# Optimization experiments

Hardware: AMD Instinct MI355X
Metric: run time of the kernel (lower is better)

## Reference

```python
import jax, jax.numpy as jnp
import numpy as np
from jax import lax

DIM = 256
HEAD_DIM = 64          # v head dim and hedgehog dim
HEAD_DIM_QK = 64       # must equal HEAD_DIM for the module to run
NH = DIM // HEAD_DIM   # 4
EPS = 1e-6


def setup_inputs() -> dict:
    key = jax.random.key(0)
    ks = jax.random.split(key, 12)
    B, C, H, W, D = 1, DIM, 16, 16, 16
    x = jax.random.normal(ks[0], (B, C, H, W, D), dtype=jnp.float32)
    qk_dim = HEAD_DIM_QK * NH
    # 1x1x1 conv weights for q, k (qkv_bias=False)
    Wq = jax.random.normal(ks[1], (qk_dim, C), dtype=jnp.float32) * 0.02
    Wk = jax.random.normal(ks[2], (qk_dim, C), dtype=jnp.float32) * 0.02
    # depthwise 3x3x3 conv for v (groups=dim, bias=True)
    Wv = jax.random.normal(ks[3], (C, 1, 3, 3, 3), dtype=jnp.float32) * 0.1
    bv = jax.random.normal(ks[4], (C,), dtype=jnp.float32) * 0.02
    # HedgeHog linear layers (init is identity/zeros; use near-identity + noise)
    eye = jnp.eye(HEAD_DIM, dtype=jnp.float32)
    Wmq = eye * 0.5 + jax.random.normal(ks[5], (HEAD_DIM, HEAD_DIM), dtype=jnp.float32) * 0.02
    bmq = jnp.zeros((HEAD_DIM,), dtype=jnp.float32)
    Wmk = eye * 0.5 + jax.random.normal(ks[6], (HEAD_DIM, HEAD_DIM), dtype=jnp.float32) * 0.02
    bmk = jnp.zeros((HEAD_DIM,), dtype=jnp.float32)
    Wmv = eye * 0.5 + jax.random.normal(ks[7], (HEAD_DIM, HEAD_DIM), dtype=jnp.float32) * 0.02
    bmv = jnp.zeros((HEAD_DIM,), dtype=jnp.float32)
    return {"x": x, "Wq": Wq, "Wk": Wk, "Wv": Wv, "bv": bv,
            "Wmq": Wmq, "bmq": bmq, "Wmk": Wmk, "bmk": bmk,
            "Wmv": Wmv, "bmv": bmv}


def _hedgehog(z, W, b):
    # z: [B, nh, N, d] -> [B, 2*nh, N, d]; cat along HEAD axis (dim=1) as in torch code
    h = jnp.einsum('bhnd,ed->bhne', z, W) + b
    return jnp.concatenate([jnp.exp(h), jnp.exp(-h)], axis=1)


def reference(x, Wq, Wk, Wv, bv, Wmq, bmq, Wmk, bmk, Wmv, bmv):
    B, C, H, W_, D = x.shape
    N = H * W_ * D
    x2 = x.reshape(B, C, N)
    # 1x1x1 conv projections
    q = jnp.einsum('oc,bcn->bon', Wq, x2)  # [B, qk_dim, N]
    k = jnp.einsum('oc,bcn->bon', Wk, x2)
    # depthwise 3x3x3 conv for v
    v3 = lax.conv_general_dilated(
        x, Wv, window_strides=(1, 1, 1),
        padding=((1, 1), (1, 1), (1, 1)),
        dimension_numbers=('NCDHW', 'OIDHW', 'NCDHW'),
        feature_group_count=C) + bv[None, :, None, None, None]
    v = v3.reshape(B, C, N)
    # split heads, tokens-last -> tokens axis
    q1 = q.reshape(B, NH, HEAD_DIM_QK, N).transpose(0, 1, 3, 2)  # [B,nh,N,dqk]
    k1 = k.reshape(B, NH, HEAD_DIM_QK, N).transpose(0, 1, 3, 2)
    v1 = v.reshape(B, NH, HEAD_DIM, N).transpose(0, 1, 3, 2)     # [B,nh,N,dv]
    qf = _hedgehog(q1, Wmq, bmq)  # [B,2nh,N,dqk]
    kf = _hedgehog(k1, Wmk, bmk)
    vf = _hedgehog(v1, Wmv, bmv)  # [B,2nh,N,dv]
    # quadratic "linear" attention: row-sum normalized QK^T
    qk = jnp.einsum('bhmd,bhnd->bhmn', qf, kf)          # [B,2nh,N,N]
    attn = qk / (jnp.sum(qk, axis=-1, keepdims=True) + EPS)
    out = jnp.einsum('bhmn,bhnd->bhmd', attn, vf)        # [B,2nh,N,dv]
    out = out.transpose(0, 1, 3, 2).reshape(B, 2 * C, H, W_, D)
    return out
```

## Files before the change

### kernel.cpp

```cpp
#include <hip/hip_runtime.h>
#include <math.h>

#define EPS_F 1e-6f

#define OFF_WCQ 0
#define OFF_WCK (OFF_WCQ + 65536)
#define OFF_BV  (OFF_WCK + 65536)
#define OFF_VC  (OFF_BV + 256)
#define OFF_PS  (OFF_VC + 256*4096)
#define OFF_PSV (OFF_PS + 8*64*4096)
#define OFF_SM  (OFF_PSV + 8*64*64)
#define OFF_SV  (OFF_SM + 8*4096)

__global__ __launch_bounds__(256) void k_combine(
    const float* __restrict__ Wq, const float* __restrict__ Wk,
    const float* __restrict__ Wmq, const float* __restrict__ Wmk,
    const float* __restrict__ Wmv, const float* __restrict__ bmv,
    const float* __restrict__ bv, float* __restrict__ ws)
{
    int row = blockIdx.x;
    int c = threadIdx.x;
    int h = row >> 6, e = row & 63;
    float aq = 0.f, ak = 0.f;
    for (int d = 0; d < 64; ++d) {
        float mq = Wmq[e*64 + d];
        float mk = Wmk[e*64 + d];
        int src = (h*64 + d)*256 + c;
        aq = fmaf(mq, Wq[src], aq);
        ak = fmaf(mk, Wk[src], ak);
    }
    ws[OFF_WCQ + row*256 + c] = aq;
    ws[OFF_WCK + row*256 + c] = ak;
    if (c == 0) {
        float av = 0.f;
        for (int d = 0; d < 64; ++d) av = fmaf(Wmv[e*64 + d], bv[h*64 + d], av);
        ws[OFF_BV + row] = av + bmv[e];
    }
}

__global__ __launch_bounds__(256) void k_dwconv(
    const float* __restrict__ x, const float* __restrict__ Wv, float* __restrict__ vc)
{
    int c = blockIdx.y;
    int n = blockIdx.x * 256 + threadIdx.x;
    int z = n >> 8, y = (n >> 4) & 15, xx = n & 15;
    const float* xc = x + c * 4096;
    const float* wc = Wv + c * 27;
    float acc = 0.f;
    #pragma unroll
    for (int kz = 0; kz < 3; ++kz) {
        int zz = z + kz - 1;
        if (zz < 0 || zz > 15) continue;
        #pragma unroll
        for (int ky = 0; ky < 3; ++ky) {
            int yy = y + ky - 1;
            if (yy < 0 || yy > 15) continue;
            #pragma unroll
            for (int kx = 0; kx < 3; ++kx) {
                int xv = xx + kx - 1;
                if (xv < 0 || xv > 15) continue;
                acc = fmaf(wc[(kz*3 + ky)*3 + kx], xc[(zz << 8) + (yy << 4) + xv], acc);
            }
        }
    }
    vc[c*4096 + n] = acc;
}

__global__ __launch_bounds__(256, 1) void k_kv_fused(
    const float* __restrict__ X, const float* __restrict__ bmk,
    const float* __restrict__ Wmv, float* __restrict__ ws)
{
    __shared__ float smem[16384];
    float (*Xs)[64]  = (float(*)[64])smem;
    float (*Ws)[68]  = (float(*)[68])(smem + 4096);
    float (*kfp)[64] = (float(*)[64])smem;
    float (*kfm)[64] = (float(*)[64])(smem + 4096);
    float (*vfp)[64] = (float(*)[64])(smem + 8192);
    float (*vfm)[64] = (float(*)[64])(smem + 12288);

    int t = threadIdx.x;
    int chunk = blockIdx.x;
    int hb = blockIdx.y;
    int n0 = chunk * 64;
    int lc = t >> 6, ln = t & 63;
    int e4 = (t & 15) * 4;
    int n4 = (t >> 4) * 4;

    float accK[4][4], accV[4][4];
    #pragma unroll
    for (int i = 0; i < 4; ++i)
        #pragma unroll
        for (int j = 0; j < 4; ++j) { accK[i][j] = 0.f; accV[i][j] = 0.f; }

    const float* Wck = ws + OFF_WCK;
    for (int c0 = 0; c0 < 256; c0 += 64) {
        #pragma unroll
        for (int i = 0; i < 16; ++i)
            Xs[lc*16 + i][ln] = X[(size_t)(c0 + lc*16 + i)*4096 + n0 + ln];
        #pragma unroll
        for (int i = 0; i < 16; ++i)
            Ws[ln][lc*16 + i] = Wck[(size_t)(hb*64 + lc*16 + i)*256 + c0 + ln];
        __syncthreads();
        #pragma unroll 4
        for (int c = 0; c < 64; ++c) {
            float4 xv4 = *(const float4*)&Xs[c][n4];
            float4 wv4 = *(const float4*)&Ws[c][e4];
            float xv[4] = {xv4.x, xv4.y, xv4.z, xv4.w};
            float wv[4] = {wv4.x, wv4.y, wv4.z, wv4.w};
            #pragma unroll
            for (int ii = 0; ii < 4; ++ii)
                #pragma unroll
                for (int jj = 0; jj < 4; ++jj)
                    accK[ii][jj] = fmaf(xv[ii], wv[jj], accK[ii][jj]);
        }
        __syncthreads();
    }

    const float* vcb = ws + OFF_VC + (size_t)hb*64*4096;
    #pragma unroll
    for (int i = 0; i < 16; ++i)
        Xs[lc*16 + i][ln] = vcb[(size_t)(lc*16 + i)*4096 + n0 + ln];
    #pragma unroll
    for (int i = 0; i < 16; ++i) { int idx = i*256 + t; Ws[idx & 63][idx >> 6] = Wmv[idx]; }
    __syncthreads();
    #pragma unroll 4
    for (int d = 0; d < 64; ++d) {
        float4 xv4 = *(const float4*)&Xs[d][n4];
        float4 wv4 = *(const float4*)&Ws[d][e4];
        float xv[4] = {xv4.x, xv4.y, xv4.z, xv4.w};
        float wv[4] = {wv4.x, wv4.y, wv4.z, wv4.w};
        #pragma unroll
        for (int ii = 0; ii < 4; ++ii)
            #pragma unroll
            for (int jj = 0; jj < 4; ++jj)
                accV[ii][jj] = fmaf(xv[ii], wv[jj], accV[ii][jj]);
    }
    __syncthreads();

    float bk[4], bvv[4];
    #pragma unroll
    for (int j = 0; j < 4; ++j) { bk[j] = bmk[e4 + j]; bvv[j] = ws[OFF_BV + hb*64 + e4 + j]; }
    #pragma unroll
    for (int ii = 0; ii < 4; ++ii) {
        float pk[4], mk_[4], pv[4], mv[4];
        #pragma unroll
        for (int jj = 0; jj < 4; ++jj) {
            float a = accK[ii][jj] + bk[jj];
            pk[jj] = __expf(a);  mk_[jj] = __expf(-a);
            float b = accV[ii][jj] + bvv[jj];
            pv[jj] = __expf(b);  mv[jj] = __expf(-b);
        }
        *(float4*)&kfp[n4 + ii][e4] = make_float4(pk[0], pk[1], pk[2], pk[3]);
        *(float4*)&kfm[n4 + ii][e4] = make_float4(mk_[0], mk_[1], mk_[2], mk_[3]);
        *(float4*)&vfp[n4 + ii][e4] = make_float4(pv[0], pv[1], pv[2], pv[3]);
        *(float4*)&vfm[n4 + ii][e4] = make_float4(mv[0], mv[1], mv[2], mv[3]);
    }
    __syncthreads();

    float aSp[4][4], aSm[4][4], svp[4], svm[4];
    #pragma unroll
    for (int i = 0; i < 4; ++i) {
        svp[i] = 0.f; svm[i] = 0.f;
        #pragma unroll
        for (int j = 0; j < 4; ++j) { aSp[i][j] = 0.f; aSm[i][j] = 0.f; }
    }
    int a4 = e4, f4 = n4;
    #pragma unroll 2
    for (int n = 0; n < 64; ++n) {
        float4 kp4 = *(const float4*)&kfp[n][a4];
        float4 km4 = *(const float4*)&kfm[n][a4];
        float4 vp4 = *(const float4*)&vfp[n][f4];
        float4 vm4 = *(const float4*)&vfm[n][f4];
        float kp[4] = {kp4.x, kp4.y, kp4.z, kp4.w};
        float km[4] = {km4.x, km4.y, km4.z, km4.w};
        float vp[4] = {vp4.x, vp4.y, vp4.z, vp4.w};
        float vm[4] = {vm4.x, vm4.y, vm4.z, vm4.w};
        #pragma unroll
        for (int ai = 0; ai < 4; ++ai) {
            svp[ai] += kp[ai];  svm[ai] += km[ai];
            #pragma unroll
            for (int fi = 0; fi < 4; ++fi) {
                aSp[ai][fi] = fmaf(kp[ai], vp[fi], aSp[ai][fi]);
                aSm[ai][fi] = fmaf(km[ai], vm[fi], aSm[ai][fi]);
            }
        }
    }
    float* pSp = ws + OFF_PS + (size_t)(hb*64 + chunk)*4096;
    float* pSm = ws + OFF_PS + (size_t)((hb + 4)*64 + chunk)*4096;
    #pragma unroll
    for (int ai = 0; ai < 4; ++ai) {
        *(float4*)&pSp[(a4 + ai)*64 + f4] = make_float4(aSp[ai][0], aSp[ai][1], aSp[ai][2], aSp[ai][3]);
        *(float4*)&pSm[(a4 + ai)*64 + f4] = make_float4(aSm[ai][0], aSm[ai][1], aSm[ai][2], aSm[ai][3]);
    }
    if (t < 16) {
        float* pvp = ws + OFF_PSV + (size_t)(hb*64 + chunk)*64;
        float* pvm = ws + OFF_PSV + (size_t)((hb + 4)*64 + chunk)*64;
        *(float4*)&pvp[a4] = make_float4(svp[0], svp[1], svp[2], svp[3]);
        *(float4*)&pvm[a4] = make_float4(svm[0], svm[1], svm[2], svm[3]);
    }
}

__global__ __launch_bounds__(256) void k_reduce(float* __restrict__ ws)
{
    int idx = blockIdx.x*256 + threadIdx.x;
    if (idx < 8*4096) {
        int h = idx >> 12, r = idx & 4095;
        float s = 0.f;
        #pragma unroll 16
        for (int c = 0; c < 64; ++c) s += ws[OFF_PS + (size_t)(h*64 + c)*4096 + r];
        ws[OFF_SM + idx] = s;
    } else if (idx < 8*4096 + 512) {
        int j = idx - 8*4096;
        int h = j >> 6, e = j & 63;
        float s = 0.f;
        #pragma unroll 16
        for (int c = 0; c < 64; ++c) s += ws[OFF_PSV + (size_t)(h*64 + c)*64 + e];
        ws[OFF_SV + j] = s;
    }
}

__global__ __launch_bounds__(256, 1) void k_q_out(
    const float* __restrict__ X, const float* __restrict__ bmq,
    const float* __restrict__ ws, float* __restrict__ out)
{
    __shared__ float smem[12352];
    float (*Xs)[64]   = (float(*)[64])smem;
    float (*Wsh)[68]  = (float(*)[68])(smem + 4096);
    float (*qfTp)[64] = (float(*)[64])smem;
    float (*qfTm)[64] = (float(*)[64])(smem + 4096);
    float (*Sms)[64]  = (float(*)[64])(smem + 8192);
    float* svs        = smem + 12288;

    int t = threadIdx.x;
    int chunk = blockIdx.x;
    int hb = blockIdx.y;
    int n0 = chunk * 64;
    int lc = t >> 6, ln = t & 63;
    int a4_1 = (t & 15) * 4;
    int n4_1 = (t >> 4) * 4;

    float accQ[4][4];
    #pragma unroll
    for (int i = 0; i < 4; ++i)
        #pragma unroll
        for (int j = 0; j < 4; ++j) accQ[i][j] = 0.f;

    const float* Wcq = ws + OFF_WCQ;
    for (int c0 = 0; c0 < 256; c0 += 64) {
        #pragma unroll
        for (int i = 0; i < 16; ++i)
            Xs[lc*16 + i][ln] = X[(size_t)(c0 + lc*16 + i)*4096 + n0 + ln];
        #pragma unroll
        for (int i = 0; i < 16; ++i)
            Wsh[ln][lc*16 + i] = Wcq[(size_t)(hb*64 + lc*16 + i)*256 + c0 + ln];
        __syncthreads();
        #pragma unroll 4
        for (int c = 0; c < 64; ++c) {
            float4 xv4 = *(const float4*)&Xs[c][n4_1];
            float4 wv4 = *(const float4*)&Wsh[c][a4_1];
            float xv[4] = {xv4.x, xv4.y, xv4.z, xv4.w};
            float wv[4] = {wv4.x, wv4.y, wv4.z, wv4.w};
            #pragma unroll
            for (int ii = 0; ii < 4; ++ii)
                #pragma unroll
                for (int jj = 0; jj < 4; ++jj)
                    accQ[ii][jj] = fmaf(xv[ii], wv[jj], accQ[ii][jj]);
        }
        __syncthreads();
    }

    #pragma unroll
    for (int jj = 0; jj < 4; ++jj) {
        float b = bmq[a4_1 + jj];
        float v0 = accQ[0][jj] + b, v1 = accQ[1][jj] + b,
              v2 = accQ[2][jj] + b, v3 = accQ[3][jj] + b;
        *(float4*)&qfTp[a4_1 + jj][n4_1] =
            make_float4(__expf(v0), __expf(v1), __expf(v2), __expf(v3));
        *(float4*)&qfTm[a4_1 + jj][n4_1] =
            make_float4(__expf(-v0), __expf(-v1), __expf(-v2), __expf(-v3));
    }

    int n4 = (t & 15) * 4;
    int e4 = (t >> 4) * 4;
    for (int s = 0; s < 2; ++s) {
        int h = hb + 4*s;
        __syncthreads();
        const float* Smg = ws + OFF_SM + (size_t)h*4096;
        #pragma unroll
        for (int i = 0; i < 16; ++i) { int idx = i*256 + t; Sms[idx >> 6][idx & 63] = Smg[idx]; }
        if (t < 64) svs[t] = ws[OFF_SV + h*64 + t];
        __syncthreads();

        const float (*qf)[64] = s ? (const float(*)[64])qfTm : (const float(*)[64])qfTp;
        float acc[4][4];
        float den[4] = {0.f, 0.f, 0.f, 0.f};
        #pragma unroll
        for (int i = 0; i < 4; ++i)
            #pragma unroll
            for (int j = 0; j < 4; ++j) acc[i][j] = 0.f;
        #pragma unroll 4
        for (int a = 0; a < 64; ++a) {
            float4 qv4 = *(const float4*)&qf[a][n4];
            float4 sm4 = *(const float4*)&Sms[a][e4];
            float qv[4] = {qv4.x, qv4.y, qv4.z, qv4.w};
            float sm[4] = {sm4.x, sm4.y, sm4.z, sm4.w};
            float sva = svs[a];
            #pragma unroll
            for (int nj = 0; nj < 4; ++nj) {
                den[nj] = fmaf(qv[nj], sva, den[nj]);
                #pragma unroll
                for (int ei = 0; ei < 4; ++ei)
                    acc[ei][nj] = fmaf(sm[ei], qv[nj], acc[ei][nj]);
            }
        }
        float r[4];
        #pragma unroll
        for (int nj = 0; nj < 4; ++nj) r[nj] = 1.f / (den[nj] + EPS_F);
        #pragma unroll
        for (int ei = 0; ei < 4; ++ei)
            *(float4*)&out[(size_t)(h*64 + e4 + ei)*4096 + n0 + n4] =
                make_float4(acc[ei][0]*r[0], acc[ei][1]*r[1], acc[ei][2]*r[2], acc[ei][3]*r[3]);
    }
}

extern "C" void kernel_launch(void* const* d_in, const int* in_sizes, int n_in,
                              void* d_out, int out_size, void* d_ws, size_t ws_size,
                              hipStream_t stream) {
    const float* x   = (const float*)d_in[0];
    const float* Wq  = (const float*)d_in[1];
    const float* Wk  = (const float*)d_in[2];
    const float* Wv  = (const float*)d_in[3];
    const float* bv  = (const float*)d_in[4];
    const float* Wmq = (const float*)d_in[5];
    const float* bmq = (const float*)d_in[6];
    const float* Wmk = (const float*)d_in[7];
    const float* bmk = (const float*)d_in[8];
    const float* Wmv = (const float*)d_in[9];
    const float* bmv = (const float*)d_in[10];
    float* out = (float*)d_out;
    float* ws  = (float*)d_ws;

    k_combine<<<256, 256, 0, stream>>>(Wq, Wk, Wmq, Wmk, Wmv, bmv, bv, ws);
    k_dwconv<<<dim3(16, 256), 256, 0, stream>>>(x, Wv, ws + OFF_VC);
    k_kv_fused<<<dim3(64, 4), 256, 0, stream>>>(x, bmk, Wmv, ws);
    k_reduce<<<130, 256, 0, stream>>>(ws);
    k_q_out<<<dim3(64, 4), 256, 0, stream>>>(x, bmq, ws, out);
}
```

Measured before the change: 147.0 us.

## Halve token chunk to double block count and stage dwconv planes in LDS

The token chunk per block in the KV and Q/output kernels drops from 64 to 32, doubling the grid to 128x4 blocks. Thread tiles and shared-memory layouts are reworked to match, with padded 68-wide rows and the min-blocks launch bound removed. The depthwise conv now stages three z-planes in shared memory and uses branchless clamped reads. The aim is to fill more of the many CUs, since 256 blocks underuse the GPU. In exchange the reduce kernel sums twice as many partial S matrices, and each block gets less register reuse.

```diff
diff --git a/kernel.cpp b/kernel.cpp
--- a/kernel.cpp
+++ b/kernel.cpp
@@ -2,14 +2,15 @@
 #include <math.h>
 
 #define EPS_F 1e-6f
+#define NCHUNK 128
 
 #define OFF_WCQ 0
 #define OFF_WCK (OFF_WCQ + 65536)
 #define OFF_BV  (OFF_WCK + 65536)
 #define OFF_VC  (OFF_BV + 256)
 #define OFF_PS  (OFF_VC + 256*4096)
-#define OFF_PSV (OFF_PS + 8*64*4096)
-#define OFF_SM  (OFF_PSV + 8*64*64)
+#define OFF_PSV (OFF_PS + 8*NCHUNK*4096)
+#define OFF_SM  (OFF_PSV + 8*NCHUNK*64)
 #define OFF_SV  (OFF_SM + 8*4096)
 
 __global__ __launch_bounds__(256) void k_combine(
@@ -41,74 +42,85 @@
 __global__ __launch_bounds__(256) void k_dwconv(
     const float* __restrict__ x, const float* __restrict__ Wv, float* __restrict__ vc)
 {
+    __shared__ float pl[3][256];
+    int t = threadIdx.x;
+    int z = blockIdx.x;
     int c = blockIdx.y;
-    int n = blockIdx.x * 256 + threadIdx.x;
-    int z = n >> 8, y = (n >> 4) & 15, xx = n & 15;
-    const float* xc = x + c * 4096;
-    const float* wc = Wv + c * 27;
-    float acc = 0.f;
+    const float* xc = x + (size_t)c*4096;
     #pragma unroll
     for (int kz = 0; kz < 3; ++kz) {
         int zz = z + kz - 1;
-        if (zz < 0 || zz > 15) continue;
+        pl[kz][t] = (zz >= 0 && zz < 16) ? xc[zz*256 + t] : 0.f;
+    }
+    __syncthreads();
+    int y = t >> 4, xx = t & 15;
+    const float* wc = Wv + c*27;
+    float acc = 0.f;
+    #pragma unroll
+    for (int kz = 0; kz < 3; ++kz) {
         #pragma unroll
         for (int ky = 0; ky < 3; ++ky) {
             int yy = y + ky - 1;
-            if (yy < 0 || yy > 15) continue;
+            bool vy = (yy >= 0) && (yy < 16);
+            int yc = yy < 0 ? 0 : (yy > 15 ? 15 : yy);
             #pragma unroll
             for (int kx = 0; kx < 3; ++kx) {
                 int xv = xx + kx - 1;
-                if (xv < 0 || xv > 15) continue;
-                acc = fmaf(wc[(kz*3 + ky)*3 + kx], xc[(zz << 8) + (yy << 4) + xv], acc);
+                bool v = vy && (xv >= 0) && (xv < 16);
+                int xc2 = xv < 0 ? 0 : (xv > 15 ? 15 : xv);
+                float val = pl[kz][yc*16 + xc2];
+                acc = fmaf(wc[(kz*3 + ky)*3 + kx], v ? val : 0.f, acc);
             }
         }
     }
-    vc[c*4096 + n] = acc;
-}
-
-__global__ __launch_bounds__(256, 1) void k_kv_fused(
+    vc[(size_t)c*4096 + z*256 + t] = acc;
+}
+
+__global__ __launch_bounds__(256) void k_kv_fused(
     const float* __restrict__ X, const float* __restrict__ bmk,
     const float* __restrict__ Wmv, float* __restrict__ ws)
 {
-    __shared__ float smem[16384];
-    float (*Xs)[64]  = (float(*)[64])smem;
-    float (*Ws)[68]  = (float(*)[68])(smem + 4096);
-    float (*kfp)[64] = (float(*)[64])smem;
-    float (*kfm)[64] = (float(*)[64])(smem + 4096);
-    float (*vfp)[64] = (float(*)[64])(smem + 8192);
-    float (*vfm)[64] = (float(*)[64])(smem + 12288);
+    __shared__ float smem[8704];
+    float* Xs  = smem;
+    float* Wsh = smem + 2048;
+    float* kfp = smem;
+    float* kfm = smem + 2176;
+    float* vfp = smem + 4352;
+    float* vfm = smem + 6528;
 
     int t = threadIdx.x;
     int chunk = blockIdx.x;
     int hb = blockIdx.y;
-    int n0 = chunk * 64;
+    int n0 = chunk * 32;
+    int e4 = (t & 15) * 4;
+    int n2 = (t >> 4) * 2;
     int lc = t >> 6, ln = t & 63;
-    int e4 = (t & 15) * 4;
-    int n4 = (t >> 4) * 4;
-
-    float accK[4][4], accV[4][4];
-    #pragma unroll
-    for (int i = 0; i < 4; ++i)
+
+    float accK[2][4], accV[2][4];
+    #pragma unroll
+    for (int i = 0; i < 2; ++i)
         #pragma unroll
         for (int j = 0; j < 4; ++j) { accK[i][j] = 0.f; accV[i][j] = 0.f; }
 
     const float* Wck = ws + OFF_WCK;
     for (int c0 = 0; c0 < 256; c0 += 64) {
         #pragma unroll
+        for (int i = 0; i < 8; ++i) {
+            int idx = i*256 + t, cc = idx >> 5, nn = idx & 31;
+            Xs[cc*32 + nn] = X[(size_t)(c0 + cc)*4096 + n0 + nn];
+        }
+        #pragma unroll
         for (int i = 0; i < 16; ++i)
-            Xs[lc*16 + i][ln] = X[(size_t)(c0 + lc*16 + i)*4096 + n0 + ln];
-        #pragma unroll
-        for (int i = 0; i < 16; ++i)
-            Ws[ln][lc*16 + i] = Wck[(size_t)(hb*64 + lc*16 + i)*256 + c0 + ln];
-        __syncthreads();
-        #pragma unroll 4
+            Wsh[ln*68 + lc*16 + i] = Wck[(size_t)(hb*64 + lc*16 + i)*256 + c0 + ln];
+        __syncthreads();
+        #pragma unroll 8
         for (int c = 0; c < 64; ++c) {
-            float4 xv4 = *(const float4*)&Xs[c][n4];
-            float4 wv4 = *(const float4*)&Ws[c][e4];
-            float xv[4] = {xv4.x, xv4.y, xv4.z, xv4.w};
+            float2 xv2 = *(const float2*)&Xs[c*32 + n2];
+            float4 wv4 = *(const float4*)&Wsh[c*68 + e4];
+            float xv[2] = {xv2.x, xv2.y};
             float wv[4] = {wv4.x, wv4.y, wv4.z, wv4.w};
             #pragma unroll
-            for (int ii = 0; ii < 4; ++ii)
+            for (int ii = 0; ii < 2; ++ii)
                 #pragma unroll
                 for (int jj = 0; jj < 4; ++jj)
                     accK[ii][jj] = fmaf(xv[ii], wv[jj], accK[ii][jj]);
@@ -116,32 +128,39 @@
         __syncthreads();
     }
 
-    const float* vcb = ws + OFF_VC + (size_t)hb*64*4096;
-    #pragma unroll
-    for (int i = 0; i < 16; ++i)
-        Xs[lc*16 + i][ln] = vcb[(size_t)(lc*16 + i)*4096 + n0 + ln];
-    #pragma unroll
-    for (int i = 0; i < 16; ++i) { int idx = i*256 + t; Ws[idx & 63][idx >> 6] = Wmv[idx]; }
-    __syncthreads();
-    #pragma unroll 4
-    for (int d = 0; d < 64; ++d) {
-        float4 xv4 = *(const float4*)&Xs[d][n4];
-        float4 wv4 = *(const float4*)&Ws[d][e4];
-        float xv[4] = {xv4.x, xv4.y, xv4.z, xv4.w};
-        float wv[4] = {wv4.x, wv4.y, wv4.z, wv4.w};
-        #pragma unroll
-        for (int ii = 0; ii < 4; ++ii)
-            #pragma unroll
-            for (int jj = 0; jj < 4; ++jj)
-                accV[ii][jj] = fmaf(xv[ii], wv[jj], accV[ii][jj]);
-    }
-    __syncthreads();
+    {
+        const float* vcb = ws + OFF_VC + (size_t)hb*64*4096;
+        #pragma unroll
+        for (int i = 0; i < 8; ++i) {
+            int idx = i*256 + t, dd = idx >> 5, nn = idx & 31;
+            Xs[dd*32 + nn] = vcb[(size_t)dd*4096 + n0 + nn];
+        }
+        #pragma unroll
+        for (int i = 0; i < 16; ++i) {
+            int idx = i*256 + t, dd = idx & 63, ee = idx >> 6;
+            Wsh[dd*68 + ee] = Wmv[ee*64 + dd];
+        }
+        __syncthreads();
+        #pragma unroll 8
+        for (int d = 0; d < 64; ++d) {
+            float2 xv2 = *(const float2*)&Xs[d*32 + n2];
+            float4 wv4 = *(const float4*)&Wsh[d*68 + e4];
+            float xv[2] = {xv2.x, xv2.y};
+            float wv[4] = {wv4.x, wv4.y, wv4.z, wv4.w};
+            #pragma unroll
+            for (int ii = 0; ii < 2; ++ii)
+                #pragma unroll
+                for (int jj = 0; jj < 4; ++jj)
+                    accV[ii][jj] = fmaf(xv[ii], wv[jj], accV[ii][jj]);
+        }
+        __syncthreads();
+    }
 
     float bk[4], bvv[4];
     #pragma unroll
     for (int j = 0; j < 4; ++j) { bk[j] = bmk[e4 + j]; bvv[j] = ws[OFF_BV + hb*64 + e4 + j]; }
     #pragma unroll
-    for (int ii = 0; ii < 4; ++ii) {
+    for (int ii = 0; ii < 2; ++ii) {
         float pk[4], mk_[4], pv[4], mv[4];
         #pragma unroll
         for (int jj = 0; jj < 4; ++jj) {
@@ -150,13 +169,15 @@
             float b = accV[ii][jj] + bvv[jj];
             pv[jj] = __expf(b);  mv[jj] = __expf(-b);
         }
-        *(float4*)&kfp[n4 + ii][e4] = make_float4(pk[0], pk[1], pk[2], pk[3]);
-        *(float4*)&kfm[n4 + ii][e4] = make_float4(mk_[0], mk_[1], mk_[2], mk_[3]);
-        *(float4*)&vfp[n4 + ii][e4] = make_float4(pv[0], pv[1], pv[2], pv[3]);
-        *(float4*)&vfm[n4 + ii][e4] = make_float4(mv[0], mv[1], mv[2], mv[3]);
+        int r = (n2 + ii)*68 + e4;
+        *(float4*)&kfp[r] = make_float4(pk[0], pk[1], pk[2], pk[3]);
+        *(float4*)&kfm[r] = make_float4(mk_[0], mk_[1], mk_[2], mk_[3]);
+        *(float4*)&vfp[r] = make_float4(pv[0], pv[1], pv[2], pv[3]);
+        *(float4*)&vfm[r] = make_float4(mv[0], mv[1], mv[2], mv[3]);
     }
     __syncthreads();
 
+    int a4 = e4, f4 = (t >> 4) * 4;
     float aSp[4][4], aSm[4][4], svp[4], svm[4];
     #pragma unroll
     for (int i = 0; i < 4; ++i) {
@@ -164,13 +185,12 @@
         #pragma unroll
         for (int j = 0; j < 4; ++j) { aSp[i][j] = 0.f; aSm[i][j] = 0.f; }
     }
-    int a4 = e4, f4 = n4;
-    #pragma unroll 2
-    for (int n = 0; n < 64; ++n) {
-        float4 kp4 = *(const float4*)&kfp[n][a4];
-        float4 km4 = *(const float4*)&kfm[n][a4];
-        float4 vp4 = *(const float4*)&vfp[n][f4];
-        float4 vm4 = *(const float4*)&vfm[n][f4];
+    #pragma unroll 4
+    for (int n = 0; n < 32; ++n) {
+        float4 kp4 = *(const float4*)&kfp[n*68 + a4];
+        float4 km4 = *(const float4*)&kfm[n*68 + a4];
+        float4 vp4 = *(const float4*)&vfp[n*68 + f4];
+        float4 vm4 = *(const float4*)&vfm[n*68 + f4];
         float kp[4] = {kp4.x, kp4.y, kp4.z, kp4.w};
         float km[4] = {km4.x, km4.y, km4.z, km4.w};
         float vp[4] = {vp4.x, vp4.y, vp4.z, vp4.w};
@@ -185,16 +205,16 @@
             }
         }
     }
-    float* pSp = ws + OFF_PS + (size_t)(hb*64 + chunk)*4096;
-    float* pSm = ws + OFF_PS + (size_t)((hb + 4)*64 + chunk)*4096;
+    float* pSp = ws + OFF_PS + (size_t)(hb*NCHUNK + chunk)*4096;
+    float* pSm = ws + OFF_PS + (size_t)((hb + 4)*NCHUNK + chunk)*4096;
     #pragma unroll
     for (int ai = 0; ai < 4; ++ai) {
         *(float4*)&pSp[(a4 + ai)*64 + f4] = make_float4(aSp[ai][0], aSp[ai][1], aSp[ai][2], aSp[ai][3]);
         *(float4*)&pSm[(a4 + ai)*64 + f4] = make_float4(aSm[ai][0], aSm[ai][1], aSm[ai][2], aSm[ai][3]);
     }
     if (t < 16) {
-        float* pvp = ws + OFF_PSV + (size_t)(hb*64 + chunk)*64;
-        float* pvm = ws + OFF_PSV + (size_t)((hb + 4)*64 + chunk)*64;
+        float* pvp = ws + OFF_PSV + (size_t)(hb*NCHUNK + chunk)*64;
+        float* pvm = ws + OFF_PSV + (size_t)((hb + 4)*NCHUNK + chunk)*64;
         *(float4*)&pvp[a4] = make_float4(svp[0], svp[1], svp[2], svp[3]);
         *(float4*)&pvm[a4] = make_float4(svm[0], svm[1], svm[2], svm[3]);
     }
@@ -206,120 +226,121 @@
     if (idx < 8*4096) {
         int h = idx >> 12, r = idx & 4095;
         float s = 0.f;
-        #pragma unroll 16
-        for (int c = 0; c < 64; ++c) s += ws[OFF_PS + (size_t)(h*64 + c)*4096 + r];
+        #pragma unroll 8
+        for (int c = 0; c < NCHUNK; ++c) s += ws[OFF_PS + (size_t)(h*NCHUNK + c)*4096 + r];
         ws[OFF_SM + idx] = s;
     } else if (idx < 8*4096 + 512) {
         int j = idx - 8*4096;
         int h = j >> 6, e = j & 63;
         float s = 0.f;
-        #pragma unroll 16
-        for (int c = 0; c < 64; ++c) s += ws[OFF_PSV + (size_t)(h*64 + c)*64 + e];
+        #pragma unroll 8
+        for (int c = 0; c < NCHUNK; ++c) s += ws[OFF_PSV + (size_t)(h*NCHUNK + c)*64 + e];
         ws[OFF_SV + j] = s;
     }
 }
 
-__global__ __launch_bounds__(256, 1) void k_q_out(
+__global__ __launch_bounds__(256) void k_q_out(
     const float* __restrict__ X, const float* __restrict__ bmq,
     const float* __restrict__ ws, float* __restrict__ out)
 {
-    __shared__ float smem[12352];
-    float (*Xs)[64]   = (float(*)[64])smem;
-    float (*Wsh)[68]  = (float(*)[68])(smem + 4096);
-    float (*qfTp)[64] = (float(*)[64])smem;
-    float (*qfTm)[64] = (float(*)[64])(smem + 4096);
-    float (*Sms)[64]  = (float(*)[64])(smem + 8192);
-    float* svs        = smem + 12288;
+    __shared__ float smem[8768];
+    float* Xs  = smem;
+    float* Wsh = smem + 2048;
+    float* qfp = smem;
+    float* qfm = smem + 2176;
+    float* Sms = smem + 4352;
+    float* svs = smem + 8704;
 
     int t = threadIdx.x;
     int chunk = blockIdx.x;
     int hb = blockIdx.y;
-    int n0 = chunk * 64;
+    int n0 = chunk * 32;
+    int e2 = (t & 31) * 2;
+    int n4 = (t >> 5) * 4;
     int lc = t >> 6, ln = t & 63;
-    int a4_1 = (t & 15) * 4;
-    int n4_1 = (t >> 4) * 4;
-
-    float accQ[4][4];
-    #pragma unroll
-    for (int i = 0; i < 4; ++i)
-        #pragma unroll
-        for (int j = 0; j < 4; ++j) accQ[i][j] = 0.f;
+
+    float accQ[4][2];
+    #pragma unroll
+    for (int i = 0; i < 4; ++i) { accQ[i][0] = 0.f; accQ[i][1] = 0.f; }
 
     const float* Wcq = ws + OFF_WCQ;
     for (int c0 = 0; c0 < 256; c0 += 64) {
         #pragma unroll
+        for (int i = 0; i < 8; ++i) {
+            int idx = i*256 + t, cc = idx >> 5, nn = idx & 31;
+            Xs[cc*32 + nn] = X[(size_t)(c0 + cc)*4096 + n0 + nn];
+        }
+        #pragma unroll
         for (int i = 0; i < 16; ++i)
-            Xs[lc*16 + i][ln] = X[(size_t)(c0 + lc*16 + i)*4096 + n0 + ln];
-        #pragma unroll
-        for (int i = 0; i < 16; ++i)
-            Wsh[ln][lc*16 + i] = Wcq[(size_t)(hb*64 + lc*16 + i)*256 + c0 + ln];
-        __syncthreads();
-        #pragma unroll 4
+            Wsh[ln*68 + lc*16 + i] = Wcq[(size_t)(hb*64 + lc*16 + i)*256 + c0 + ln];
+        __syncthreads();
+        #pragma unroll 8
         for (int c = 0; c < 64; ++c) {
-            float4 xv4 = *(const float4*)&Xs[c][n4_1];
-            float4 wv4 = *(const float4*)&Wsh[c][a4_1];
+            float4 xv4 = *(const float4*)&Xs[c*32 + n4];
+            float2 wv2 = *(const float2*)&Wsh[c*68 + e2];
             float xv[4] = {xv4.x, xv4.y, xv4.z, xv4.w};
-            float wv[4] = {wv4.x, wv4.y, wv4.z, wv4.w};
+            float wv[2] = {wv2.x, wv2.y};
             #pragma unroll
             for (int ii = 0; ii < 4; ++ii)
                 #pragma unroll
-                for (int jj = 0; jj < 4; ++jj)
+                for (int jj = 0; jj < 2; ++jj)
                     accQ[ii][jj] = fmaf(xv[ii], wv[jj], accQ[ii][jj]);
         }
         __syncthreads();
     }
 
-    #pragma unroll
-    for (int jj = 0; jj < 4; ++jj) {
-        float b = bmq[a4_1 + jj];
-        float v0 = accQ[0][jj] + b, v1 = accQ[1][jj] + b,
-              v2 = accQ[2][jj] + b, v3 = accQ[3][jj] + b;
-        *(float4*)&qfTp[a4_1 + jj][n4_1] =
-            make_float4(__expf(v0), __expf(v1), __expf(v2), __expf(v3));
-        *(float4*)&qfTm[a4_1 + jj][n4_1] =
-            make_float4(__expf(-v0), __expf(-v1), __expf(-v2), __expf(-v3));
-    }
-
-    int n4 = (t & 15) * 4;
-    int e4 = (t >> 4) * 4;
+    float bq[2] = {bmq[e2], bmq[e2 + 1]};
+    #pragma unroll
+    for (int ii = 0; ii < 4; ++ii) {
+        float a0 = accQ[ii][0] + bq[0];
+        float a1 = accQ[ii][1] + bq[1];
+        int r = (n4 + ii)*68 + e2;
+        *(float2*)&qfp[r] = make_float2(__expf(a0),  __expf(a1));
+        *(float2*)&qfm[r] = make_float2(__expf(-a0), __expf(-a1));
+    }
+
     for (int s = 0; s < 2; ++s) {
         int h = hb + 4*s;
         __syncthreads();
         const float* Smg = ws + OFF_SM + (size_t)h*4096;
         #pragma unroll
-        for (int i = 0; i < 16; ++i) { int idx = i*256 + t; Sms[idx >> 6][idx & 63] = Smg[idx]; }
+        for (int i = 0; i < 16; ++i) {
+            int idx = i*256 + t;
+            Sms[(idx >> 6)*68 + (idx & 63)] = Smg[idx];
+        }
         if (t < 64) svs[t] = ws[OFF_SV + h*64 + t];
         __syncthreads();
 
-        const float (*qf)[64] = s ? (const float(*)[64])qfTm : (const float(*)[64])qfTp;
-        float acc[4][4];
+        const float* qf = s ? qfm : qfp;
+        float accO[2][4];
         float den[4] = {0.f, 0.f, 0.f, 0.f};
         #pragma unroll
-        for (int i = 0; i < 4; ++i)
-            #pragma unroll
-            for (int j = 0; j < 4; ++j) acc[i][j] = 0.f;
+        for (int j = 0; j < 2; ++j)
+            #pragma unroll
+            for (int i = 0; i < 4; ++i) accO[j][i] = 0.f;
         #pragma unroll 4
         for (int a = 0; a < 64; ++a) {
-            float4 qv4 = *(const float4*)&qf[a][n4];
-            float4 sm4 = *(const float4*)&Sms[a][e4];
-            float qv[4] = {qv4.x, qv4.y, qv4.z, qv4.w};
-            float sm[4] = {sm4.x, sm4.y, sm4.z, sm4.w};
             float sva = svs[a];
-            #pragma unroll
-            for (int nj = 0; nj < 4; ++nj) {
-                den[nj] = fmaf(qv[nj], sva, den[nj]);
+            float2 sm2 = *(const float2*)&Sms[a*68 + e2];
+            float sm[2] = {sm2.x, sm2.y};
+            float qv[4];
+            #pragma unroll
+            for (int i = 0; i < 4; ++i) qv[i] = qf[(n4 + i)*68 + a];
+            #pragma unroll
+            for (int i = 0; i < 4; ++i) {
+                den[i] = fmaf(qv[i], sva, den[i]);
                 #pragma unroll
-                for (int ei = 0; ei < 4; ++ei)
-                    acc[ei][nj] = fmaf(sm[ei], qv[nj], acc[ei][nj]);
+                for (int j = 0; j < 2; ++j)
+                    accO[j][i] = fmaf(sm[j], qv[i], accO[j][i]);
             }
         }
         float r[4];
         #pragma unroll
-        for (int nj = 0; nj < 4; ++nj) r[nj] = 1.f / (den[nj] + EPS_F);
-        #pragma unroll
-        for (int ei = 0; ei < 4; ++ei)
-            *(float4*)&out[(size_t)(h*64 + e4 + ei)*4096 + n0 + n4] =
-                make_float4(acc[ei][0]*r[0], acc[ei][1]*r[1], acc[ei][2]*r[2], acc[ei][3]*r[3]);
+        for (int i = 0; i < 4; ++i) r[i] = 1.f / (den[i] + EPS_F);
+        #pragma unroll
+        for (int j = 0; j < 2; ++j)
+            *(float4*)&out[(size_t)(h*64 + e2 + j)*4096 + n0 + n4] =
+                make_float4(accO[j][0]*r[0], accO[j][1]*r[1], accO[j][2]*r[2], accO[j][3]*r[3]);
     }
 }
 
@@ -342,7 +363,7 @@
 
     k_combine<<<256, 256, 0, stream>>>(Wq, Wk, Wmq, Wmk, Wmv, bmv, bv, ws);
     k_dwconv<<<dim3(16, 256), 256, 0, stream>>>(x, Wv, ws + OFF_VC);
-    k_kv_fused<<<dim3(64, 4), 256, 0, stream>>>(x, bmk, Wmv, ws);
+    k_kv_fused<<<dim3(NCHUNK, 4), 256, 0, stream>>>(x, bmk, Wmv, ws);
     k_reduce<<<130, 256, 0, stream>>>(ws);
-    k_q_out<<<dim3(64, 4), 256, 0, stream>>>(x, bmq, ws, out);
-}
+    k_q_out<<<dim3(NCHUNK, 4), 256, 0, stream>>>(x, bmq, ws, out);
+}
```

Measured after the change: 150.6 us. +2.5%, slower.

## Merge prep kernels, replace partial-sum reduce with atomics, tile dwconv in LDS

Applied to the files above, without the earlier changes.

Merges the weight-combine and depthwise-conv kernels into one launch. The conv now stages three z-planes in shared memory. It also zeroes the S/sv accumulators. The kv kernel now atomically adds its per-chunk partial state into the global S and sv buffers, so the separate reduce kernel and its large partial-sum buffer are gone. The q/out kernel drops launch_bounds min-occupancy, prefetches S before the Q projection and reads sv from global memory. This cuts two launches and a memory round trip, but adds heavy atomic contention (64 chunks per element) and makes the float summation order nondeterministic.

```diff
diff --git a/kernel.cpp b/kernel.cpp
--- a/kernel.cpp
+++ b/kernel.cpp
@@ -7,76 +7,82 @@
 #define OFF_WCK (OFF_WCQ + 65536)
 #define OFF_BV  (OFF_WCK + 65536)
 #define OFF_VC  (OFF_BV + 256)
-#define OFF_PS  (OFF_VC + 256*4096)
-#define OFF_PSV (OFF_PS + 8*64*4096)
-#define OFF_SM  (OFF_PSV + 8*64*64)
+#define OFF_SM  (OFF_VC + 256*4096)
 #define OFF_SV  (OFF_SM + 8*4096)
 
-__global__ __launch_bounds__(256) void k_combine(
+__global__ __launch_bounds__(256) void k_prep(
+    const float* __restrict__ x,  const float* __restrict__ Wv,
     const float* __restrict__ Wq, const float* __restrict__ Wk,
     const float* __restrict__ Wmq, const float* __restrict__ Wmk,
     const float* __restrict__ Wmv, const float* __restrict__ bmv,
     const float* __restrict__ bv, float* __restrict__ ws)
 {
-    int row = blockIdx.x;
-    int c = threadIdx.x;
-    int h = row >> 6, e = row & 63;
-    float aq = 0.f, ak = 0.f;
-    for (int d = 0; d < 64; ++d) {
-        float mq = Wmq[e*64 + d];
-        float mk = Wmk[e*64 + d];
-        int src = (h*64 + d)*256 + c;
-        aq = fmaf(mq, Wq[src], aq);
-        ak = fmaf(mk, Wk[src], ak);
-    }
-    ws[OFF_WCQ + row*256 + c] = aq;
-    ws[OFF_WCK + row*256 + c] = ak;
-    if (c == 0) {
-        float av = 0.f;
-        for (int d = 0; d < 64; ++d) av = fmaf(Wmv[e*64 + d], bv[h*64 + d], av);
-        ws[OFF_BV + row] = av + bmv[e];
+    int b = blockIdx.x, t = threadIdx.x;
+    if (b < 256) {
+        int gid = b*256 + t;
+        if (gid < 8*4096 + 512) ws[OFF_SM + gid] = 0.f;
+        int h = b >> 6, e = b & 63;
+        float aq = 0.f, ak = 0.f;
+        for (int d = 0; d < 64; ++d) {
+            float mq = Wmq[e*64 + d];
+            float mk = Wmk[e*64 + d];
+            int src = (h*64 + d)*256 + t;
+            aq = fmaf(mq, Wq[src], aq);
+            ak = fmaf(mk, Wk[src], ak);
+        }
+        ws[OFF_WCQ + b*256 + t] = aq;
+        ws[OFF_WCK + b*256 + t] = ak;
+        if (t == 0) {
+            float av = 0.f;
+            for (int d = 0; d < 64; ++d) av = fmaf(Wmv[e*64 + d], bv[h*64 + d], av);
+            ws[OFF_BV + b] = av + bmv[e];
+        }
+    } else {
+        __shared__ float pl[3][256];
+        int bb = b - 256;
+        int z = bb & 15, c = bb >> 4;
+        const float* xc = x + (size_t)c*4096;
+        #pragma unroll
+        for (int kz = 0; kz < 3; ++kz) {
+            int zz = z + kz - 1;
+            pl[kz][t] = (zz >= 0 && zz < 16) ? xc[zz*256 + t] : 0.f;
+        }
+        __syncthreads();
+        int y = t >> 4, xx = t & 15;
+        const float* wc = Wv + c*27;
+        float acc = 0.f;
+        #pragma unroll
+        for (int kz = 0; kz < 3; ++kz) {
+            #pragma unroll
+            for (int ky = 0; ky < 3; ++ky) {
+                int yy = y + ky - 1;
+                bool vy = (yy >= 0) && (yy < 16);
+                int yc = yy < 0 ? 0 : (yy > 15 ? 15 : yy);
+                #pragma unroll
+                for (int kx = 0; kx < 3; ++kx) {
+                    int xv = xx + kx - 1;
+                    bool v = vy && (xv >= 0) && (xv < 16);
+                    int xc2 = xv < 0 ? 0 : (xv > 15 ? 15 : xv);
+                    float val = pl[kz][yc*16 + xc2];
+                    acc = fmaf(wc[(kz*3 + ky)*3 + kx], v ? val : 0.f, acc);
+                }
+            }
+        }
+        ws[OFF_VC + (size_t)c*4096 + z*256 + t] = acc;
     }
 }
 
-__global__ __launch_bounds__(256) void k_dwconv(
-    const float* __restrict__ x, const float* __restrict__ Wv, float* __restrict__ vc)
-{
-    int c = blockIdx.y;
-    int n = blockIdx.x * 256 + threadIdx.x;
-    int z = n >> 8, y = (n >> 4) & 15, xx = n & 15;
-    const float* xc = x + c * 4096;
-    const float* wc = Wv + c * 27;
-    float acc = 0.f;
-    #pragma unroll
-    for (int kz = 0; kz < 3; ++kz) {
-        int zz = z + kz - 1;
-        if (zz < 0 || zz > 15) continue;
-        #pragma unroll
-        for (int ky = 0; ky < 3; ++ky) {
-            int yy = y + ky - 1;
-            if (yy < 0 || yy > 15) continue;
-            #pragma unroll
-            for (int kx = 0; kx < 3; ++kx) {
-                int xv = xx + kx - 1;
-                if (xv < 0 || xv > 15) continue;
-                acc = fmaf(wc[(kz*3 + ky)*3 + kx], xc[(zz << 8) + (yy << 4) + xv], acc);
-            }
-        }
-    }
-    vc[c*4096 + n] = acc;
-}
-
-__global__ __launch_bounds__(256, 1) void k_kv_fused(
+__global__ __launch_bounds__(256) void k_kv(
     const float* __restrict__ X, const float* __restrict__ bmk,
     const float* __restrict__ Wmv, float* __restrict__ ws)
 {
     __shared__ float smem[16384];
-    float (*Xs)[64]  = (float(*)[64])smem;
-    float (*Ws)[68]  = (float(*)[68])(smem + 4096);
-    float (*kfp)[64] = (float(*)[64])smem;
-    float (*kfm)[64] = (float(*)[64])(smem + 4096);
-    float (*vfp)[64] = (float(*)[64])(smem + 8192);
-    float (*vfm)[64] = (float(*)[64])(smem + 12288);
+    float* Xs  = smem;
+    float* Wsh = smem + 4096;
+    float* kfp = smem;
+    float* kfm = smem + 4096;
+    float* vfp = smem + 8192;
+    float* vfm = smem + 12288;
 
     int t = threadIdx.x;
     int chunk = blockIdx.x;
@@ -96,15 +102,15 @@
     for (int c0 = 0; c0 < 256; c0 += 64) {
         #pragma unroll
         for (int i = 0; i < 16; ++i)
-            Xs[lc*16 + i][ln] = X[(size_t)(c0 + lc*16 + i)*4096 + n0 + ln];
-        #pragma unroll
-        for (int i = 0; i < 16; ++i)
-            Ws[ln][lc*16 + i] = Wck[(size_t)(hb*64 + lc*16 + i)*256 + c0 + ln];
+            Xs[(lc*16 + i)*64 + ln] = X[(size_t)(c0 + lc*16 + i)*4096 + n0 + ln];
+        #pragma unroll
+        for (int i = 0; i < 16; ++i)
+            Wsh[ln*68 + lc*16 + i] = Wck[(size_t)(hb*64 + lc*16 + i)*256 + c0 + ln];
         __syncthreads();
         #pragma unroll 4
         for (int c = 0; c < 64; ++c) {
-            float4 xv4 = *(const float4*)&Xs[c][n4];
-            float4 wv4 = *(const float4*)&Ws[c][e4];
+            float4 xv4 = *(const float4*)&Xs[c*64 + n4];
+            float4 wv4 = *(const float4*)&Wsh[c*68 + e4];
             float xv[4] = {xv4.x, xv4.y, xv4.z, xv4.w};
             float wv[4] = {wv4.x, wv4.y, wv4.z, wv4.w};
             #pragma unroll
@@ -116,26 +122,31 @@
         __syncthreads();
     }
 
-    const float* vcb = ws + OFF_VC + (size_t)hb*64*4096;
-    #pragma unroll
-    for (int i = 0; i < 16; ++i)
-        Xs[lc*16 + i][ln] = vcb[(size_t)(lc*16 + i)*4096 + n0 + ln];
-    #pragma unroll
-    for (int i = 0; i < 16; ++i) { int idx = i*256 + t; Ws[idx & 63][idx >> 6] = Wmv[idx]; }
-    __syncthreads();
-    #pragma unroll 4
-    for (int d = 0; d < 64; ++d) {
-        float4 xv4 = *(const float4*)&Xs[d][n4];
-        float4 wv4 = *(const float4*)&Ws[d][e4];
-        float xv[4] = {xv4.x, xv4.y, xv4.z, xv4.w};
-        float wv[4] = {wv4.x, wv4.y, wv4.z, wv4.w};
-        #pragma unroll
-        for (int ii = 0; ii < 4; ++ii)
-            #pragma unroll
-            for (int jj = 0; jj < 4; ++jj)
-                accV[ii][jj] = fmaf(xv[ii], wv[jj], accV[ii][jj]);
-    }
-    __syncthreads();
+    {
+        const float* vcb = ws + OFF_VC + (size_t)hb*64*4096;
+        #pragma unroll
+        for (int i = 0; i < 16; ++i)
+            Xs[(lc*16 + i)*64 + ln] = vcb[(size_t)(lc*16 + i)*4096 + n0 + ln];
+        #pragma unroll
+        for (int i = 0; i < 16; ++i) {
+            int idx = i*256 + t, dd = idx & 63, ee = idx >> 6;
+            Wsh[dd*68 + ee] = Wmv[ee*64 + dd];
+        }
+        __syncthreads();
+        #pragma unroll 4
+        for (int d = 0; d < 64; ++d) {
+            float4 xv4 = *(const float4*)&Xs[d*64 + n4];
+            float4 wv4 = *(const float4*)&Wsh[d*68 + e4];
+            float xv[4] = {xv4.x, xv4.y, xv4.z, xv4.w};
+            float wv[4] = {wv4.x, wv4.y, wv4.z, wv4.w};
+            #pragma unroll
+            for (int ii = 0; ii < 4; ++ii)
+                #pragma unroll
+                for (int jj = 0; jj < 4; ++jj)
+                    accV[ii][jj] = fmaf(xv[ii], wv[jj], accV[ii][jj]);
+        }
+        __syncthreads();
+    }
 
     float bk[4], bvv[4];
     #pragma unroll
@@ -150,13 +161,15 @@
             float b = accV[ii][jj] + bvv[jj];
             pv[jj] = __expf(b);  mv[jj] = __expf(-b);
         }
-        *(float4*)&kfp[n4 + ii][e4] = make_float4(pk[0], pk[1], pk[2], pk[3]);
-        *(float4*)&kfm[n4 + ii][e4] = make_float4(mk_[0], mk_[1], mk_[2], mk_[3]);
-        *(float4*)&vfp[n4 + ii][e4] = make_float4(pv[0], pv[1], pv[2], pv[3]);
-        *(float4*)&vfm[n4 + ii][e4] = make_float4(mv[0], mv[1], mv[2], mv[3]);
+        int r = (n4 + ii)*64 + e4;
+        *(float4*)&kfp[r] = make_float4(pk[0], pk[1], pk[2], pk[3]);
+        *(float4*)&kfm[r] = make_float4(mk_[0], mk_[1], mk_[2], mk_[3]);
+        *(float4*)&vfp[r] = make_float4(pv[0], pv[1], pv[2], pv[3]);
+        *(float4*)&vfm[r] = make_float4(mv[0], mv[1], mv[2], mv[3]);
     }
     __syncthreads();
 
+    int a4 = e4, f4 = n4;
     float aSp[4][4], aSm[4][4], svp[4], svm[4];
     #pragma unroll
     for (int i = 0; i < 4; ++i) {
@@ -164,13 +177,12 @@
         #pragma unroll
         for (int j = 0; j < 4; ++j) { aSp[i][j] = 0.f; aSm[i][j] = 0.f; }
     }
-    int a4 = e4, f4 = n4;
     #pragma unroll 2
     for (int n = 0; n < 64; ++n) {
-        float4 kp4 = *(const float4*)&kfp[n][a4];
-        float4 km4 = *(const float4*)&kfm[n][a4];
-        float4 vp4 = *(const float4*)&vfp[n][f4];
-        float4 vm4 = *(const float4*)&vfm[n][f4];
+        float4 kp4 = *(const float4*)&kfp[n*64 + a4];
+        float4 km4 = *(const float4*)&kfm[n*64 + a4];
+        float4 vp4 = *(const float4*)&vfp[n*64 + f4];
+        float4 vm4 = *(const float4*)&vfm[n*64 + f4];
         float kp[4] = {kp4.x, kp4.y, kp4.z, kp4.w};
         float km[4] = {km4.x, km4.y, km4.z, km4.w};
         float vp[4] = {vp4.x, vp4.y, vp4.z, vp4.w};
@@ -185,59 +197,46 @@
             }
         }
     }
-    float* pSp = ws + OFF_PS + (size_t)(hb*64 + chunk)*4096;
-    float* pSm = ws + OFF_PS + (size_t)((hb + 4)*64 + chunk)*4096;
-    #pragma unroll
-    for (int ai = 0; ai < 4; ++ai) {
-        *(float4*)&pSp[(a4 + ai)*64 + f4] = make_float4(aSp[ai][0], aSp[ai][1], aSp[ai][2], aSp[ai][3]);
-        *(float4*)&pSm[(a4 + ai)*64 + f4] = make_float4(aSm[ai][0], aSm[ai][1], aSm[ai][2], aSm[ai][3]);
-    }
+    float* Smp = ws + OFF_SM + (size_t)hb*4096;
+    float* Smm = ws + OFF_SM + (size_t)(hb + 4)*4096;
+    #pragma unroll
+    for (int ai = 0; ai < 4; ++ai)
+        #pragma unroll
+        for (int fi = 0; fi < 4; ++fi) {
+            atomicAdd(&Smp[(a4 + ai)*64 + f4 + fi], aSp[ai][fi]);
+            atomicAdd(&Smm[(a4 + ai)*64 + f4 + fi], aSm[ai][fi]);
+        }
     if (t < 16) {
-        float* pvp = ws + OFF_PSV + (size_t)(hb*64 + chunk)*64;
-        float* pvm = ws + OFF_PSV + (size_t)((hb + 4)*64 + chunk)*64;
-        *(float4*)&pvp[a4] = make_float4(svp[0], svp[1], svp[2], svp[3]);
-        *(float4*)&pvm[a4] = make_float4(svm[0], svm[1], svm[2], svm[3]);
+        #pragma unroll
+        for (int i = 0; i < 4; ++i) {
+            atomicAdd(&ws[OFF_SV + hb*64 + a4 + i], svp[i]);
+            atomicAdd(&ws[OFF_SV + (hb + 4)*64 + a4 + i], svm[i]);
+        }
     }
 }
 
-__global__ __launch_bounds__(256) void k_reduce(float* __restrict__ ws)
-{
-    int idx = blockIdx.x*256 + threadIdx.x;
-    if (idx < 8*4096) {
-        int h = idx >> 12, r = idx & 4095;
-        float s = 0.f;
-        #pragma unroll 16
-        for (int c = 0; c < 64; ++c) s += ws[OFF_PS + (size_t)(h*64 + c)*4096 + r];
-        ws[OFF_SM + idx] = s;
-    } else if (idx < 8*4096 + 512) {
-        int j = idx - 8*4096;
-        int h = j >> 6, e = j & 63;
-        float s = 0.f;
-        #pragma unroll 16
-        for (int c = 0; c < 64; ++c) s += ws[OFF_PSV + (size_t)(h*64 + c)*64 + e];
-        ws[OFF_SV + j] = s;
-    }
-}
-
-__global__ __launch_bounds__(256, 1) void k_q_out(
+__global__ __launch_bounds__(256) void k_q_out(
     const float* __restrict__ X, const float* __restrict__ bmq,
     const float* __restrict__ ws, float* __restrict__ out)
 {
-    __shared__ float smem[12352];
-    float (*Xs)[64]   = (float(*)[64])smem;
-    float (*Wsh)[68]  = (float(*)[68])(smem + 4096);
-    float (*qfTp)[64] = (float(*)[64])smem;
-    float (*qfTm)[64] = (float(*)[64])(smem + 4096);
-    float (*Sms)[64]  = (float(*)[64])(smem + 8192);
-    float* svs        = smem + 12288;
+    __shared__ float smem[12544];
+    float* Xs   = smem;
+    float* Wsh  = smem + 4096;
+    float* qfTp = smem;
+    float* qfTm = smem + 4096;
+    float* Sms  = smem + 8448;
 
     int t = threadIdx.x;
     int chunk = blockIdx.x;
     int hb = blockIdx.y;
     int n0 = chunk * 64;
     int lc = t >> 6, ln = t & 63;
-    int a4_1 = (t & 15) * 4;
-    int n4_1 = (t >> 4) * 4;
+    int a4 = (t & 15) * 4;
+    int n4 = (t >> 4) * 4;
+
+    const float* SgP = ws + OFF_SM + (size_t)hb*4096;
+    #pragma unroll
+    for (int i = 0; i < 16; ++i) { int idx = i*256 + t; Sms[idx] = SgP[idx]; }
 
     float accQ[4][4];
     #pragma unroll
@@ -249,15 +248,15 @@
     for (int c0 = 0; c0 < 256; c0 += 64) {
         #pragma unroll
         for (int i = 0; i < 16; ++i)
-            Xs[lc*16 + i][ln] = X[(size_t)(c0 + lc*16 + i)*4096 + n0 + ln];
-        #pragma unroll
-        for (int i = 0; i < 16; ++i)
-            Wsh[ln][lc*16 + i] = Wcq[(size_t)(hb*64 + lc*16 + i)*256 + c0 + ln];
+            Xs[(lc*16 + i)*64 + ln] = X[(size_t)(c0 + lc*16 + i)*4096 + n0 + ln];
+        #pragma unroll
+        for (int i = 0; i < 16; ++i)
+            Wsh[ln*68 + lc*16 + i] = Wcq[(size_t)(hb*64 + lc*16 + i)*256 + c0 + ln];
         __syncthreads();
         #pragma unroll 4
         for (int c = 0; c < 64; ++c) {
-            float4 xv4 = *(const float4*)&Xs[c][n4_1];
-            float4 wv4 = *(const float4*)&Wsh[c][a4_1];
+            float4 xv4 = *(const float4*)&Xs[c*64 + n4];
+            float4 wv4 = *(const float4*)&Wsh[c*68 + a4];
             float xv[4] = {xv4.x, xv4.y, xv4.z, xv4.w};
             float wv[4] = {wv4.x, wv4.y, wv4.z, wv4.w};
             #pragma unroll
@@ -271,27 +270,28 @@
 
     #pragma unroll
     for (int jj = 0; jj < 4; ++jj) {
-        float b = bmq[a4_1 + jj];
+        float b = bmq[a4 + jj];
         float v0 = accQ[0][jj] + b, v1 = accQ[1][jj] + b,
               v2 = accQ[2][jj] + b, v3 = accQ[3][jj] + b;
-        *(float4*)&qfTp[a4_1 + jj][n4_1] =
+        *(float4*)&qfTp[(a4 + jj)*64 + n4] =
             make_float4(__expf(v0), __expf(v1), __expf(v2), __expf(v3));
-        *(float4*)&qfTm[a4_1 + jj][n4_1] =
+        *(float4*)&qfTm[(a4 + jj)*64 + n4] =
             make_float4(__expf(-v0), __expf(-v1), __expf(-v2), __expf(-v3));
     }
 
-    int n4 = (t & 15) * 4;
-    int e4 = (t >> 4) * 4;
+    int n4b = (t & 15) * 4;
+    int e4b = (t >> 4) * 4;
     for (int s = 0; s < 2; ++s) {
         int h = hb + 4*s;
-        __syncthreads();
-        const float* Smg = ws + OFF_SM + (size_t)h*4096;
-        #pragma unroll
-        for (int i = 0; i < 16; ++i) { int idx = i*256 + t; Sms[idx >> 6][idx & 63] = Smg[idx]; }
-        if (t < 64) svs[t] = ws[OFF_SV + h*64 + t];
-        __syncthreads();
-
-        const float (*qf)[64] = s ? (const float(*)[64])qfTm : (const float(*)[64])qfTp;
+        if (s) {
+            __syncthreads();
+            const float* SgM = ws + OFF_SM + (size_t)h*4096;
+            #pragma unroll
+            for (int i = 0; i < 16; ++i) { int idx = i*256 + t; Sms[idx] = SgM[idx]; }
+        }
+        __syncthreads();
+        const float* qf  = s ? qfTm : qfTp;
+        const float* svg = ws + OFF_SV + h*64;
         float acc[4][4];
         float den[4] = {0.f, 0.f, 0.f, 0.f};
         #pragma unroll
@@ -300,11 +300,11 @@
             for (int j = 0; j < 4; ++j) acc[i][j] = 0.f;
         #pragma unroll 4
         for (int a = 0; a < 64; ++a) {
-            float4 qv4 = *(const float4*)&qf[a][n4];
-            float4 sm4 = *(const float4*)&Sms[a][e4];
+            float4 qv4 = *(const float4*)&qf[a*64 + n4b];
+            float4 sm4 = *(const float4*)&Sms[a*64 + e4b];
             float qv[4] = {qv4.x, qv4.y, qv4.z, qv4.w};
             float sm[4] = {sm4.x, sm4.y, sm4.z, sm4.w};
-            float sva = svs[a];
+            float sva = svg[a];
             #pragma unroll
             for (int nj = 0; nj < 4; ++nj) {
                 den[nj] = fmaf(qv[nj], sva, den[nj]);
@@ -318,7 +318,7 @@
         for (int nj = 0; nj < 4; ++nj) r[nj] = 1.f / (den[nj] + EPS_F);
         #pragma unroll
         for (int ei = 0; ei < 4; ++ei)
-            *(float4*)&out[(size_t)(h*64 + e4 + ei)*4096 + n0 + n4] =
+            *(float4*)&out[(size_t)(h*64 + e4b + ei)*4096 + n0 + n4b] =
                 make_float4(acc[ei][0]*r[0], acc[ei][1]*r[1], acc[ei][2]*r[2], acc[ei][3]*r[3]);
     }
 }
@@ -340,9 +340,7 @@
     float* out = (float*)d_out;
     float* ws  = (float*)d_ws;
 
-    k_combine<<<256, 256, 0, stream>>>(Wq, Wk, Wmq, Wmk, Wmv, bmv, bv, ws);
-    k_dwconv<<<dim3(16, 256), 256, 0, stream>>>(x, Wv, ws + OFF_VC);
-    k_kv_fused<<<dim3(64, 4), 256, 0, stream>>>(x, bmk, Wmv, ws);
-    k_reduce<<<130, 256, 0, stream>>>(ws);
+    k_prep<<<4352, 256, 0, stream>>>(x, Wv, Wq, Wk, Wmq, Wmk, Wmv, bmv, bv, ws);
+    k_kv<<<dim3(64, 4), 256, 0, stream>>>(x, bmk, Wmv, ws);
     k_q_out<<<dim3(64, 4), 256, 0, stream>>>(x, bmq, ws, out);
 }
```

New measurement: 161.0 us. 1.1x slower.
